# Kernel optimization log

Measured on AMD Instinct MI355X. Metric: run time of the kernel, lower is better.

Reference implementation:

```python
import jax, jax.numpy as jnp
import numpy as np

V_SRC = 32000
V_TRG = 32000
E = 512
H = 512


def _lstm(emb, Wih, Whh, bih, bhh, h0, c0):
    # emb: [S,E]; Wih: [4H,E]; Whh: [4H,H]; PyTorch gate order i,f,g,o
    pre = emb @ Wih.T + (bih + bhh)  # [S,4H]

    def step(carry, x):
        h, c = carry
        g = x + h @ Whh.T
        i, f, gg, o = jnp.split(g, 4)
        i = jax.nn.sigmoid(i)
        f = jax.nn.sigmoid(f)
        gg = jnp.tanh(gg)
        o = jax.nn.sigmoid(o)
        c = f * c + i * gg
        h = o * jnp.tanh(c)
        return (h, c), h

    (h, c), hs = jax.lax.scan(step, (h0, c0), pre)
    return hs, (h, c)


def setup_inputs() -> dict:
    key = jax.random.key(0)
    ks = jax.random.split(key, 16)
    sd_e = 1.0 / np.sqrt(H)
    inp = {
        "source": jax.random.randint(ks[0], (512,), 0, V_SRC),
        "target": jax.random.randint(ks[1], (512,), 0, V_TRG),
        # encoder params (embedding init uniform(-0.25,0.25) as in source)
        "enc_embed": jax.random.uniform(ks[2], (V_SRC, E), jnp.float32, -0.25, 0.25),
        "enc_Wih": jax.random.uniform(ks[3], (4 * H, E), jnp.float32, -sd_e, sd_e),
        "enc_Whh": jax.random.uniform(ks[4], (4 * H, H), jnp.float32, -sd_e, sd_e),
        "enc_bih": jax.random.uniform(ks[5], (4 * H,), jnp.float32, -sd_e, sd_e),
        "enc_bhh": jax.random.uniform(ks[6], (4 * H,), jnp.float32, -sd_e, sd_e),
        # decoder params
        "dec_embed": jax.random.normal(ks[7], (V_TRG, E), jnp.float32),
        "dec_Wih": jax.random.uniform(ks[8], (4 * H, E), jnp.float32, -sd_e, sd_e),
        "dec_Whh": jax.random.uniform(ks[9], (4 * H, H), jnp.float32, -sd_e, sd_e),
        "dec_bih": jax.random.uniform(ks[10], (4 * H,), jnp.float32, -sd_e, sd_e),
        "dec_bhh": jax.random.uniform(ks[11], (4 * H,), jnp.float32, -sd_e, sd_e),
        "W_out": jax.random.uniform(ks[12], (V_TRG, H), jnp.float32, -sd_e, sd_e),
        "b_out": jax.random.uniform(ks[13], (V_TRG,), jnp.float32, -sd_e, sd_e),
    }
    return inp


def reference(source, target, enc_embed, enc_Wih, enc_Whh, enc_bih, enc_bhh,
              dec_embed, dec_Wih, dec_Whh, dec_bih, dec_bhh, W_out, b_out):
    # Encoder: run LSTM over source tokens, keep final (h, c)
    src_emb = enc_embed[source]  # [S,E]
    h0 = jnp.zeros((H,), src_emb.dtype)
    c0 = jnp.zeros((H,), src_emb.dtype)
    _, (h, c) = _lstm(src_emb, enc_Wih, enc_Whh, enc_bih, enc_bhh, h0, c0)

    # Decoder: teacher-forced, one LSTM step per target token (target[:-1] in, target[1:] out)
    trg_in = target[:-1]
    trg_out = target[1:]
    dec_emb = dec_embed[trg_in]  # [T-1,E]
    hs, _ = _lstm(dec_emb, dec_Wih, dec_Whh, dec_bih, dec_bhh, h, c)  # [T-1,H]
    logits = hs @ W_out.T + b_out  # [T-1,V]
    logp = jax.nn.log_softmax(logits, axis=-1)
    # per-step CrossEntropyLoss (batch of 1 each step -> just the NLL of the gold token)
    losses = -jnp.take_along_axis(logp, trg_out[:, None], axis=1)[:, 0]  # [T-1]
    return losses
```

## Files before the change

kernel.cpp:

```cpp
#include <hip/hip_runtime.h>

#define UNROLL _Pragma("unroll")

typedef __attribute__((ext_vector_type(8))) short bf16x8;
typedef __attribute__((ext_vector_type(4))) float f32x4;

__device__ __forceinline__ unsigned short f2bf_rne(float x) {
  unsigned u = __float_as_uint(x);
  unsigned r = (u + 0x7FFFu + ((u >> 16) & 1u)) >> 16;
  return (unsigned short)r;
}

__device__ __forceinline__ float fast_sigmoid(float x) {
  return __builtin_amdgcn_rcpf(1.f + __expf(-x));
}
__device__ __forceinline__ float fast_tanh(float x) {
  return 1.f - 2.f * __builtin_amdgcn_rcpf(__expf(2.f * x) + 1.f);
}

__global__ void k_init(unsigned long long* hword) {
  int t = threadIdx.x;
  for (int i = t; i < 8192; i += 256) hword[i] = 0ull;
}

__global__ __launch_bounds__(512, 1) void k_lstm(
    const int* __restrict__ source, const int* __restrict__ target,
    const float* __restrict__ enc_embed, const float* __restrict__ enc_Wih,
    const float* __restrict__ enc_Whh, const float* __restrict__ enc_bih,
    const float* __restrict__ enc_bhh, const float* __restrict__ dec_embed,
    const float* __restrict__ dec_Wih, const float* __restrict__ dec_Whh,
    const float* __restrict__ dec_bih, const float* __restrict__ dec_bhh,
    unsigned long long* hword, unsigned short* hsb) {
  const int blk = blockIdx.x;
  const int tid = threadIdx.x;
  const int lane = tid & 63;
  const int wv = tid >> 6;
  const int U = (blk << 3) + wv;
  const int mycopy = blk & 7;

  __shared__ int toks[1024];
  __shared__ float hsm[2][512];
  toks[tid] = source[tid];
  toks[512 + tid] = target[tid];
  __syncthreads();

  float c = 0.f;

  for (int phase = 0; phase < 2; ++phase) {
    const float* emb = phase ? dec_embed : enc_embed;
    const float* Wih = phase ? dec_Wih : enc_Wih;
    const float* Whh = phase ? dec_Whh : enc_Whh;
    const float* bih = phase ? dec_bih : enc_bih;
    const float* bhh = phase ? dec_bhh : enc_bhh;

    float wih[4][8], whh[4][8], bias[4];
    UNROLL for (int g = 0; g < 4; ++g) {
      const float* p1 = Wih + (size_t)((g << 9) + U) * 512 + lane;
      const float* p2 = Whh + (size_t)((g << 9) + U) * 512 + lane;
      UNROLL for (int k = 0; k < 8; ++k) { wih[g][k] = p1[k << 6]; whh[g][k] = p2[k << 6]; }
      bias[g] = bih[(g << 9) + U] + bhh[(g << 9) + U];
    }
    UNROLL for (int g = 0; g < 4; ++g) UNROLL for (int k = 0; k < 8; ++k) {
      asm volatile("" : "+v"(wih[g][k]));
      asm volatile("" : "+v"(whh[g][k]));
    }

    const int T = phase ? 511 : 512;
    const int tko = phase ? 512 : 0;
    for (int t = 0; t < T; ++t) {
      const int S = (phase ? 512 : 0) + t;
      const int par = S & 1;

      const float* ep = emb + (size_t)toks[tko + t] * 512 + lane;
      float ev[8];
      UNROLL for (int k = 0; k < 8; ++k) ev[k] = ep[k << 6];
      float acc[4];
      UNROLL for (int g = 0; g < 4; ++g) {
        float a = 0.f;
        UNROLL for (int k = 0; k < 8; ++k) a += wih[g][k] * ev[k];
        acc[g] = a;
      }
      UNROLL for (int g = 0; g < 4; ++g) asm volatile("" : "+v"(acc[g]));

      if (S > 0) {
        const unsigned long long* hw = hword + (mycopy << 10) + (par << 9) + (wv << 6) + lane;
        unsigned long long w;
        do {
          w = __hip_atomic_load(hw, __ATOMIC_RELAXED, __HIP_MEMORY_SCOPE_AGENT);
        } while (!__all((unsigned)(w >> 32) == (unsigned)S));
        hsm[par][(wv << 6) + lane] = __uint_as_float((unsigned)w);
      }
      __syncthreads();
      float hv[8];
      if (S > 0) {
        UNROLL for (int k = 0; k < 8; ++k) hv[k] = hsm[par][(k << 6) + lane];
      } else {
        UNROLL for (int k = 0; k < 8; ++k) hv[k] = 0.f;
      }

      UNROLL for (int g = 0; g < 4; ++g) {
        float a = acc[g];
        UNROLL for (int k = 0; k < 8; ++k) a += whh[g][k] * hv[k];
        acc[g] = a;
      }
      UNROLL for (int mask = 1; mask < 64; mask <<= 1) {
        UNROLL for (int g = 0; g < 4; ++g) acc[g] += __shfl_xor(acc[g], mask, 64);
      }
      float ia = fast_sigmoid(acc[0] + bias[0]);
      float fa = fast_sigmoid(acc[1] + bias[1]);
      float ga = fast_tanh(acc[2] + bias[2]);
      float oa = fast_sigmoid(acc[3] + bias[3]);
      c = fa * c + ia * ga;
      float h = oa * fast_tanh(c);

      if (lane == 0) {
        unsigned long long w =
            ((unsigned long long)(unsigned)(S + 1) << 32) | (unsigned long long)__float_as_uint(h);
        const int dst = (((S + 1) & 1) << 9) + U;
        UNROLL for (int cp = 0; cp < 8; ++cp)
          __hip_atomic_store(&hword[(cp << 10) + dst], w, __ATOMIC_RELAXED,
                             __HIP_MEMORY_SCOPE_AGENT);
        if (phase) hsb[((size_t)t << 9) + U] = f2bf_rne(h);
      }
    }
  }
}

__global__ __launch_bounds__(256, 2) void k_logits(
    const unsigned short* __restrict__ hsb, const float* __restrict__ W_out,
    const float* __restrict__ b_out, const int* __restrict__ target,
    float* __restrict__ pmax, float* __restrict__ psum, float* __restrict__ tgt) {
  const int nt = blockIdx.x;
  const int mt = blockIdx.y;
  const int nbase = nt << 7;
  const int mbase = mt << 7;
  const int tid = threadIdx.x;
  const int l = tid & 63;
  const int q = l >> 4;
  const int cc = l & 15;
  const int W = tid >> 6;
  const int wm = W >> 1, wn = W & 1;

  __shared__ __align__(16) unsigned short Asm[128][40];
  __shared__ __align__(16) unsigned short Bsm[128][40];
  __shared__ float ex[2][128][2];

  f32x4 acc[4][4];
  f32x4 zero = {0.f, 0.f, 0.f, 0.f};
  UNROLL for (int i = 0; i < 4; ++i) UNROLL for (int j = 0; j < 4; ++j) acc[i][j] = zero;

  const int srow = tid >> 1;
  const int sh = tid & 1;

  for (int kc = 0; kc < 16; ++kc) {
    const unsigned short* ap = hsb + (size_t)(mbase + srow) * 512 + (kc << 5) + (sh << 4);
    uint4 a0 = *(const uint4*)ap;
    uint4 a1 = *(const uint4*)(ap + 8);
    *(uint4*)&Asm[srow][(sh << 4)] = a0;
    *(uint4*)&Asm[srow][(sh << 4) + 8] = a1;

    const float* bp = W_out + (size_t)(nbase + srow) * 512 + (kc << 5) + (sh << 4);
    float bv[16];
    *(float4*)&bv[0] = *(const float4*)bp;
    *(float4*)&bv[4] = *(const float4*)(bp + 4);
    *(float4*)&bv[8] = *(const float4*)(bp + 8);
    *(float4*)&bv[12] = *(const float4*)(bp + 12);
    unsigned short us[16];
    UNROLL for (int j = 0; j < 16; ++j) us[j] = f2bf_rne(bv[j]);
    *(uint4*)&Bsm[srow][(sh << 4)] = *(const uint4*)&us[0];
    *(uint4*)&Bsm[srow][(sh << 4) + 8] = *(const uint4*)&us[8];

    __syncthreads();

    bf16x8 af[4], bfr[4];
    UNROLL for (int mi = 0; mi < 4; ++mi)
      af[mi] = *(const bf16x8*)((const char*)Asm + (size_t)((wm << 6) + (mi << 4) + cc) * 80 + (q << 4));
    UNROLL for (int ni = 0; ni < 4; ++ni)
      bfr[ni] = *(const bf16x8*)((const char*)Bsm + (size_t)((wn << 6) + (ni << 4) + cc) * 80 + (q << 4));
    UNROLL for (int mi = 0; mi < 4; ++mi)
      UNROLL for (int ni = 0; ni < 4; ++ni)
        acc[mi][ni] = __builtin_amdgcn_mfma_f32_16x16x32_bf16(af[mi], bfr[ni], acc[mi][ni], 0, 0, 0);

    __syncthreads();
  }

  float bo[4];
  UNROLL for (int ni = 0; ni < 4; ++ni) bo[ni] = b_out[nbase + (wn << 6) + (ni << 4) + cc];
  UNROLL for (int mi = 0; mi < 4; ++mi)
    UNROLL for (int ni = 0; ni < 4; ++ni)
      UNROLL for (int r = 0; r < 4; ++r) acc[mi][ni][r] += bo[ni];

  UNROLL for (int mi = 0; mi < 4; ++mi) {
    UNROLL for (int r = 0; r < 4; ++r) {
      float v0 = acc[mi][0][r], v1 = acc[mi][1][r], v2 = acc[mi][2][r], v3 = acc[mi][3][r];
      float m = fmaxf(fmaxf(v0, v1), fmaxf(v2, v3));
      m = fmaxf(m, __shfl_xor(m, 1));
      m = fmaxf(m, __shfl_xor(m, 2));
      m = fmaxf(m, __shfl_xor(m, 4));
      m = fmaxf(m, __shfl_xor(m, 8));
      float s = __expf(v0 - m) + __expf(v1 - m) + __expf(v2 - m) + __expf(v3 - m);
      s += __shfl_xor(s, 1);
      s += __shfl_xor(s, 2);
      s += __shfl_xor(s, 4);
      s += __shfl_xor(s, 8);
      int rowb = (wm << 6) + (mi << 4) + (q << 2) + r;
      if (cc == 0) { ex[wn][rowb][0] = m; ex[wn][rowb][1] = s; }
      int t = mbase + rowb;
      if (t < 511) {
        int rel = target[t + 1] - nbase - (wn << 6);
        if (rel >= 0 && rel < 64 && (rel & 15) == cc) {
          int nisel = rel >> 4;
          float v = nisel == 0 ? v0 : (nisel == 1 ? v1 : (nisel == 2 ? v2 : v3));
          tgt[t] = v;
        }
      }
    }
  }
  __syncthreads();
  if (tid < 128) {
    int t = mbase + tid;
    if (t < 511) {
      float m0 = ex[0][tid][0], s0 = ex[0][tid][1];
      float m1 = ex[1][tid][0], s1 = ex[1][tid][1];
      float M = fmaxf(m0, m1);
      float S = s0 * __expf(m0 - M) + s1 * __expf(m1 - M);
      pmax[(nt << 9) + t] = M;
      psum[(nt << 9) + t] = S;
    }
  }
}

__global__ void k_loss(const float* __restrict__ pmax, const float* __restrict__ psum,
                       const float* __restrict__ tgt, float* __restrict__ out) {
  int t = threadIdx.x;
  if (t >= 511) return;
  float M = -3.4e38f;
  for (int nt = 0; nt < 250; ++nt) M = fmaxf(M, pmax[(nt << 9) + t]);
  float S = 0.f;
  for (int nt = 0; nt < 250; ++nt) S += psum[(nt << 9) + t] * __expf(pmax[(nt << 9) + t] - M);
  out[t] = M + logf(S) - tgt[t];
}

extern "C" void kernel_launch(void* const* d_in, const int* in_sizes, int n_in,
                              void* d_out, int out_size, void* d_ws, size_t ws_size,
                              hipStream_t stream) {
  const int* source = (const int*)d_in[0];
  const int* target = (const int*)d_in[1];
  const float* enc_embed = (const float*)d_in[2];
  const float* enc_Wih = (const float*)d_in[3];
  const float* enc_Whh = (const float*)d_in[4];
  const float* enc_bih = (const float*)d_in[5];
  const float* enc_bhh = (const float*)d_in[6];
  const float* dec_embed = (const float*)d_in[7];
  const float* dec_Wih = (const float*)d_in[8];
  const float* dec_Whh = (const float*)d_in[9];
  const float* dec_bih = (const float*)d_in[10];
  const float* dec_bhh = (const float*)d_in[11];
  const float* W_out = (const float*)d_in[12];
  const float* b_out = (const float*)d_in[13];
  float* out = (float*)d_out;

  char* ws = (char*)d_ws;
  unsigned long long* hword = (unsigned long long*)(ws + 16384);
  float* pmax = (float*)(ws + 16384);
  float* tgt = (float*)(ws + 528384);
  unsigned short* hsb = (unsigned short*)(ws + 530432);
  float* psum = (float*)(ws + 1054720);

  k_init<<<1, 256, 0, stream>>>(hword);
  k_lstm<<<64, 512, 0, stream>>>(source, target, enc_embed, enc_Wih, enc_Whh, enc_bih, enc_bhh,
                                 dec_embed, dec_Wih, dec_Whh, dec_bih, dec_bhh, hword, hsb);
  k_logits<<<dim3(250, 4), 256, 0, stream>>>(hsb, W_out, b_out, target, pmax, psum, tgt);
  k_loss<<<1, 512, 0, stream>>>(pmax, psum, tgt, out);
}
```

Measured before the change: 1.983 ms.

## Precompute input projections with MFMA GEMM and halve recurrent LSTM block count

The input-to-hidden projection (emb @ Wih + biases) for all encoder and decoder steps moves out of the serial recurrence into a separate bf16 MFMA GEMM kernel, which writes a gate-interleaved pre-activation buffer. The recurrent kernel now only does the Whh matvec. Each wave handles two hidden units, so 32 blocks replace 64, and the h broadcast stores are spread across 16 lanes instead of a serial loop in lane 0. This cuts per-step latency on the critical path at the cost of an extra launch, bf16 rounding of the input projection, and more register use per wave.

```diff
diff --git a/kernel.cpp b/kernel.cpp
--- a/kernel.cpp
+++ b/kernel.cpp
@@ -23,67 +23,146 @@
   for (int i = t; i < 8192; i += 256) hword[i] = 0ull;
 }
 
-__global__ __launch_bounds__(512, 1) void k_lstm(
+__global__ __launch_bounds__(256, 2) void k_pre(
     const int* __restrict__ source, const int* __restrict__ target,
     const float* __restrict__ enc_embed, const float* __restrict__ enc_Wih,
-    const float* __restrict__ enc_Whh, const float* __restrict__ enc_bih,
-    const float* __restrict__ enc_bhh, const float* __restrict__ dec_embed,
-    const float* __restrict__ dec_Wih, const float* __restrict__ dec_Whh,
+    const float* __restrict__ enc_bih, const float* __restrict__ enc_bhh,
+    const float* __restrict__ dec_embed, const float* __restrict__ dec_Wih,
     const float* __restrict__ dec_bih, const float* __restrict__ dec_bhh,
-    unsigned long long* hword, unsigned short* hsb) {
+    float* __restrict__ pre) {
+  const int nt = blockIdx.x;
+  const int mt = blockIdx.y;
+  const int phase = mt >> 2;
+  const int nbase = nt << 7;
+  const int mbase = mt << 7;
+  const int tid = threadIdx.x;
+  const int l = tid & 63;
+  const int q = l >> 4;
+  const int cc = l & 15;
+  const int W = tid >> 6;
+  const int wm = W >> 1, wn = W & 1;
+
+  const float* emb = phase ? dec_embed : enc_embed;
+  const float* Wih = phase ? dec_Wih : enc_Wih;
+  const float* bih = phase ? dec_bih : enc_bih;
+  const float* bhh = phase ? dec_bhh : enc_bhh;
+
+  __shared__ __align__(16) unsigned short Asm[128][40];
+  __shared__ __align__(16) unsigned short Bsm[128][40];
+
+  f32x4 acc[4][4];
+  f32x4 zero = {0.f, 0.f, 0.f, 0.f};
+  UNROLL for (int i = 0; i < 4; ++i) UNROLL for (int j = 0; j < 4; ++j) acc[i][j] = zero;
+
+  const int srow = tid >> 1;
+  const int sh = tid & 1;
+  const int m = mbase + srow;
+  int tok;
+  if (phase == 0) {
+    tok = source[m];
+  } else {
+    int rel = m - 512;
+    tok = (rel < 511) ? target[rel] : 0;
+  }
+  const float* arow = emb + (size_t)tok * 512;
+  const float* brow = Wih + (size_t)(nbase + srow) * 512;
+
+  for (int kc = 0; kc < 16; ++kc) {
+    {
+      const float* ap = arow + (kc << 5) + (sh << 4);
+      float av[16];
+      *(float4*)&av[0] = *(const float4*)ap;
+      *(float4*)&av[4] = *(const float4*)(ap + 4);
+      *(float4*)&av[8] = *(const float4*)(ap + 8);
+      *(float4*)&av[12] = *(const float4*)(ap + 12);
+      unsigned short us[16];
+      UNROLL for (int j = 0; j < 16; ++j) us[j] = f2bf_rne(av[j]);
+      *(uint4*)&Asm[srow][(sh << 4)] = *(const uint4*)&us[0];
+      *(uint4*)&Asm[srow][(sh << 4) + 8] = *(const uint4*)&us[8];
+    }
+    {
+      const float* bp = brow + (kc << 5) + (sh << 4);
+      float bv[16];
+      *(float4*)&bv[0] = *(const float4*)bp;
+      *(float4*)&bv[4] = *(const float4*)(bp + 4);
+      *(float4*)&bv[8] = *(const float4*)(bp + 8);
+      *(float4*)&bv[12] = *(const float4*)(bp + 12);
+      unsigned short us[16];
+      UNROLL for (int j = 0; j < 16; ++j) us[j] = f2bf_rne(bv[j]);
+      *(uint4*)&Bsm[srow][(sh << 4)] = *(const uint4*)&us[0];
+      *(uint4*)&Bsm[srow][(sh << 4) + 8] = *(const uint4*)&us[8];
+    }
+    __syncthreads();
+
+    bf16x8 af[4], bfr[4];
+    UNROLL for (int mi = 0; mi < 4; ++mi)
+      af[mi] = *(const bf16x8*)((const char*)Asm + (size_t)((wm << 6) + (mi << 4) + cc) * 80 + (q << 4));
+    UNROLL for (int ni = 0; ni < 4; ++ni)
+      bfr[ni] = *(const bf16x8*)((const char*)Bsm + (size_t)((wn << 6) + (ni << 4) + cc) * 80 + (q << 4));
+    UNROLL for (int mi = 0; mi < 4; ++mi)
+      UNROLL for (int ni = 0; ni < 4; ++ni)
+        acc[mi][ni] = __builtin_amdgcn_mfma_f32_16x16x32_bf16(af[mi], bfr[ni], acc[mi][ni], 0, 0, 0);
+
+    __syncthreads();
+  }
+
+  float bo[4];
+  UNROLL for (int ni = 0; ni < 4; ++ni) {
+    int cr = nbase + (wn << 6) + (ni << 4) + cc;
+    bo[ni] = bih[cr] + bhh[cr];
+  }
+  UNROLL for (int mi = 0; mi < 4; ++mi) {
+    UNROLL for (int r = 0; r < 4; ++r) {
+      int rowb = (wm << 6) + (mi << 4) + (q << 2) + r;
+      int m2 = mbase + rowb;
+      if (phase == 0 || m2 < 1023) {
+        UNROLL for (int ni = 0; ni < 4; ++ni) {
+          int cr = nbase + (wn << 6) + (ni << 4) + cc;
+          pre[(size_t)m2 * 2048 + ((cr & 511) << 2) + (cr >> 9)] = acc[mi][ni][r] + bo[ni];
+        }
+      }
+    }
+  }
+}
+
+__global__ __launch_bounds__(512, 1) void k_lstm(
+    const float* __restrict__ enc_Whh, const float* __restrict__ dec_Whh,
+    const float* __restrict__ pre, unsigned long long* hword, unsigned short* hsb) {
   const int blk = blockIdx.x;
   const int tid = threadIdx.x;
   const int lane = tid & 63;
   const int wv = tid >> 6;
-  const int U = (blk << 3) + wv;
-  const int mycopy = blk & 7;
-
-  __shared__ int toks[1024];
+  const int U0 = (blk << 4) + (wv << 1);
+  const int usel = (lane >> 3) & 1;
+  const int U = U0 + usel;
+
   __shared__ float hsm[2][512];
-  toks[tid] = source[tid];
-  toks[512 + tid] = target[tid];
-  __syncthreads();
 
   float c = 0.f;
 
   for (int phase = 0; phase < 2; ++phase) {
-    const float* emb = phase ? dec_embed : enc_embed;
-    const float* Wih = phase ? dec_Wih : enc_Wih;
     const float* Whh = phase ? dec_Whh : enc_Whh;
-    const float* bih = phase ? dec_bih : enc_bih;
-    const float* bhh = phase ? dec_bhh : enc_bhh;
-
-    float wih[4][8], whh[4][8], bias[4];
+
+    float wA[4][8], wB[4][8];
     UNROLL for (int g = 0; g < 4; ++g) {
-      const float* p1 = Wih + (size_t)((g << 9) + U) * 512 + lane;
-      const float* p2 = Whh + (size_t)((g << 9) + U) * 512 + lane;
-      UNROLL for (int k = 0; k < 8; ++k) { wih[g][k] = p1[k << 6]; whh[g][k] = p2[k << 6]; }
-      bias[g] = bih[(g << 9) + U] + bhh[(g << 9) + U];
+      const float* pA = Whh + (size_t)((g << 9) + U0) * 512 + lane;
+      const float* pB = pA + 512;
+      UNROLL for (int k = 0; k < 8; ++k) { wA[g][k] = pA[k << 6]; wB[g][k] = pB[k << 6]; }
     }
     UNROLL for (int g = 0; g < 4; ++g) UNROLL for (int k = 0; k < 8; ++k) {
-      asm volatile("" : "+v"(wih[g][k]));
-      asm volatile("" : "+v"(whh[g][k]));
+      asm volatile("" : "+v"(wA[g][k]));
+      asm volatile("" : "+v"(wB[g][k]));
     }
 
     const int T = phase ? 511 : 512;
-    const int tko = phase ? 512 : 0;
     for (int t = 0; t < T; ++t) {
       const int S = (phase ? 512 : 0) + t;
       const int par = S & 1;
 
-      const float* ep = emb + (size_t)toks[tko + t] * 512 + lane;
-      float ev[8];
-      UNROLL for (int k = 0; k < 8; ++k) ev[k] = ep[k << 6];
-      float acc[4];
-      UNROLL for (int g = 0; g < 4; ++g) {
-        float a = 0.f;
-        UNROLL for (int k = 0; k < 8; ++k) a += wih[g][k] * ev[k];
-        acc[g] = a;
-      }
-      UNROLL for (int g = 0; g < 4; ++g) asm volatile("" : "+v"(acc[g]));
+      float pf = pre[(size_t)S * 2048 + (blk << 6) + (wv << 3) + (lane & 7)];
 
       if (S > 0) {
-        const unsigned long long* hw = hword + (mycopy << 10) + (par << 9) + (wv << 6) + lane;
+        const unsigned long long* hw = hword + ((blk & 7) << 10) + (par << 9) + (wv << 6) + lane;
         unsigned long long w;
         do {
           w = __hip_atomic_load(hw, __ATOMIC_RELAXED, __HIP_MEMORY_SCOPE_AGENT);
@@ -98,30 +177,37 @@
         UNROLL for (int k = 0; k < 8; ++k) hv[k] = 0.f;
       }
 
+      float aA[4], aB[4];
       UNROLL for (int g = 0; g < 4; ++g) {
-        float a = acc[g];
-        UNROLL for (int k = 0; k < 8; ++k) a += whh[g][k] * hv[k];
-        acc[g] = a;
+        float sa = 0.f, sb = 0.f;
+        UNROLL for (int k = 0; k < 8; ++k) { sa += wA[g][k] * hv[k]; sb += wB[g][k] * hv[k]; }
+        aA[g] = sa;
+        aB[g] = sb;
       }
       UNROLL for (int mask = 1; mask < 64; mask <<= 1) {
-        UNROLL for (int g = 0; g < 4; ++g) acc[g] += __shfl_xor(acc[g], mask, 64);
-      }
-      float ia = fast_sigmoid(acc[0] + bias[0]);
-      float fa = fast_sigmoid(acc[1] + bias[1]);
-      float ga = fast_tanh(acc[2] + bias[2]);
-      float oa = fast_sigmoid(acc[3] + bias[3]);
-      c = fa * c + ia * ga;
+        UNROLL for (int g = 0; g < 4; ++g) {
+          aA[g] += __shfl_xor(aA[g], mask, 64);
+          aB[g] += __shfl_xor(aB[g], mask, 64);
+        }
+      }
+      float gsel[4];
+      UNROLL for (int g = 0; g < 4; ++g)
+        gsel[g] = (usel ? aB[g] : aA[g]) + __shfl(pf, (usel << 2) + g, 64);
+      float ia = fast_sigmoid(gsel[0]);
+      float fa = fast_sigmoid(gsel[1]);
+      float gg = fast_tanh(gsel[2]);
+      float oa = fast_sigmoid(gsel[3]);
+      c = fa * c + ia * gg;
       float h = oa * fast_tanh(c);
 
-      if (lane == 0) {
+      if (lane < 16) {
         unsigned long long w =
             ((unsigned long long)(unsigned)(S + 1) << 32) | (unsigned long long)__float_as_uint(h);
-        const int dst = (((S + 1) & 1) << 9) + U;
-        UNROLL for (int cp = 0; cp < 8; ++cp)
-          __hip_atomic_store(&hword[(cp << 10) + dst], w, __ATOMIC_RELAXED,
-                             __HIP_MEMORY_SCOPE_AGENT);
-        if (phase) hsb[((size_t)t << 9) + U] = f2bf_rne(h);
-      }
+        __hip_atomic_store(&hword[((lane & 7) << 10) + (((S + 1) & 1) << 9) + U], w,
+                           __ATOMIC_RELAXED, __HIP_MEMORY_SCOPE_AGENT);
+      }
+      if (phase && (lane == 0 || lane == 8))
+        hsb[((size_t)t << 9) + U] = f2bf_rne(h);
     }
   }
 }
@@ -261,15 +347,17 @@
   float* out = (float*)d_out;
 
   char* ws = (char*)d_ws;
-  unsigned long long* hword = (unsigned long long*)(ws + 16384);
-  float* pmax = (float*)(ws + 16384);
-  float* tgt = (float*)(ws + 528384);
-  unsigned short* hsb = (unsigned short*)(ws + 530432);
-  float* psum = (float*)(ws + 1054720);
+  unsigned long long* hword = (unsigned long long*)(ws);
+  float* tgt = (float*)(ws + 65536);
+  unsigned short* hsb = (unsigned short*)(ws + 67584);
+  float* pmax = (float*)(ws + 591872);
+  float* psum = (float*)(ws + 1116160);
+  float* pre = (float*)(ws + 1640448);
 
   k_init<<<1, 256, 0, stream>>>(hword);
-  k_lstm<<<64, 512, 0, stream>>>(source, target, enc_embed, enc_Wih, enc_Whh, enc_bih, enc_bhh,
-                                 dec_embed, dec_Wih, dec_Whh, dec_bih, dec_bhh, hword, hsb);
+  k_pre<<<dim3(16, 8), 256, 0, stream>>>(source, target, enc_embed, enc_Wih, enc_bih, enc_bhh,
+                                         dec_embed, dec_Wih, dec_bih, dec_bhh, pre);
+  k_lstm<<<32, 512, 0, stream>>>(enc_Whh, dec_Whh, pre, hword, hsb);
   k_logits<<<dim3(250, 4), 256, 0, stream>>>(hsb, W_out, b_out, target, pmax, psum, tgt);
   k_loss<<<1, 512, 0, stream>>>(pmax, psum, tgt, out);
 }
```

Measured after the change: 2.786 ms. +40.5%, slower.
